# Kernel optimization log

Hardware: AMD Instinct MI355X
Metric: run time of the kernel (lower is better)

The kernel has to match this reference:

```python
import jax, jax.numpy as jnp
import numpy as np

B, S, D = 4, 2048, 1024
P = 2
N_FEAT = 16          # n_feature_know
N_REST = 16          # n_restore_know
R = 128              # knowledge_rank
D_SPACE = 64


def setup_inputs() -> dict:
    key = jax.random.key(0)
    ks = jax.random.split(key, 6)
    x = jax.random.normal(ks[0], (B, S, D), dtype=jnp.float32)
    # per-token routing weights for each of P feature paths, in [0,1)
    feature_paths = jax.random.uniform(ks[1], (P, B, S, N_FEAT), dtype=jnp.float32)
    f_know = jax.random.normal(ks[2], (N_FEAT, D, R), dtype=jnp.float32) * 0.02
    r_know = jax.random.normal(ks[3], (N_REST, R, D), dtype=jnp.float32) * 0.02
    feature_emb = jax.random.normal(ks[4], (N_FEAT, D_SPACE), dtype=jnp.float32)
    W_router = jax.random.normal(ks[5], (D_SPACE + R, N_REST), dtype=jnp.float32) * 0.05
    return {"x": x, "feature_paths": feature_paths, "f_know": f_know,
            "r_know": r_know, "feature_emb": feature_emb, "W_router": W_router}


def reference(x, feature_paths, f_know, r_know, feature_emb, W_router):
    # Feature projection into all N low-rank banks: [B,S,N,R]
    all_h = jnp.einsum('bsd,ndr->bsnr', x, f_know)
    # Weighted sum over banks per path: [P,B,S,R]
    h_all = jnp.einsum('bsnr,pbsn->pbsr', all_h, feature_paths)
    # Context for restore routing: [P,B,S,D_SPACE]
    neuron_ctx = jnp.einsum('pbsn,nd->pbsd', feature_paths, feature_emb)
    # restore_input = cat([neuron_ctx, h]) -> router -> softmax restore weights
    restore_input = jnp.concatenate([neuron_ctx, h_all], axis=-1)  # [P,B,S,D_SPACE+R]
    logits = jnp.einsum('pbsc,cn->pbsn', restore_input, W_router)
    w = jax.nn.softmax(logits, axis=-1)                            # [P,B,S,N_REST]
    # Restore + per-token weighted combine, summed over P paths: [B,S,D]
    output = jnp.einsum('pbsr,nrd,pbsn->bsd', h_all, r_know, w)
    restore_aux_loss = jnp.float32(0.0)
    return output, restore_aux_loss
```

## Files before the change

kernel.cpp:

```cpp
#include <hip/hip_runtime.h>

typedef __attribute__((ext_vector_type(4))) float f32x4;
typedef __bf16 bf16x8 __attribute__((ext_vector_type(8)));
typedef unsigned short ushort_t;

#define T_TOK 8192
#define DIM   1024
#define NRCOL 2048

#define VMW(n)  asm volatile("s_waitcnt vmcnt(" #n ")" ::: "memory")
#define SB0()   __builtin_amdgcn_sched_barrier(0)
#define BAR()   __builtin_amdgcn_s_barrier()

static __device__ __forceinline__ unsigned short f2bf(float f) {
  unsigned int u = __builtin_bit_cast(unsigned int, f);
  u += 0x7fffu + ((u >> 16) & 1u);
  return (unsigned short)(u >> 16);
}
static __device__ __forceinline__ float bfbits2f(unsigned int lo16) {
  return __builtin_bit_cast(float, lo16 << 16);
}
static __device__ __forceinline__ void gload16(const void* g, void* l) {
  __builtin_amdgcn_global_load_lds((const __attribute__((address_space(1))) void*)g,
                                   (__attribute__((address_space(3))) void*)l, 16, 0, 0);
}

__global__ __launch_bounds__(256) void prep_kernel(const float* __restrict__ x,
                                                   const float* __restrict__ fk,
                                                   const float* __restrict__ rk,
                                                   unsigned short* __restrict__ Xbf,
                                                   unsigned short* __restrict__ W1t,
                                                   unsigned short* __restrict__ W2t) {
  const int bid = blockIdx.x, tid = threadIdx.x;
  if (bid < 2048) {
    const float4* in4 = (const float4*)x;
    uint2* o4 = (uint2*)Xbf;
    #pragma unroll
    for (int it = 0; it < 4; ++it) {
      const int i = bid * 256 + tid + it * 524288;
      float4 v = in4[i];
      uint2 o;
      o.x = (unsigned)f2bf(v.x) | ((unsigned)f2bf(v.y) << 16);
      o.y = (unsigned)f2bf(v.z) | ((unsigned)f2bf(v.w) << 16);
      o4[i] = o;
    }
    return;
  }
  __shared__ float tile[32][33];
  const float* src;
  unsigned short* dst;
  int rows, cols, r0, c0;
  if (bid < 4096) {
    const int b = bid - 2048;
    const int z = b >> 7, rem = b & 127;
    src = fk + (size_t)z * 1024 * 128;
    dst = W1t + (size_t)z * 128 * 1024;
    rows = 1024; cols = 128;
    c0 = (rem & 3) * 32; r0 = (rem >> 2) * 32;
  } else {
    const int b = bid - 4096;
    src = rk; dst = W2t;
    rows = 2048; cols = 1024;
    c0 = (b & 31) * 32; r0 = (b >> 5) * 32;
  }
  const int tx = tid & 31, ty = tid >> 5;
  #pragma unroll
  for (int i = 0; i < 32; i += 8)
    tile[ty + i][tx] = src[(size_t)(r0 + ty + i) * cols + c0 + tx];
  __syncthreads();
  #pragma unroll
  for (int i = 0; i < 32; i += 8)
    dst[(size_t)(c0 + ty + i) * rows + r0 + tx] = f2bf(tile[tx][ty + i]);
}

template<int K, bool OUT_BF16>
__global__ __launch_bounds__(256, 2) void gemmD(const ushort_t* __restrict__ A,
                                                const ushort_t* __restrict__ Bt,
                                                void* __restrict__ Cp, int N) {
  constexpr int nt = K / 64;
  __shared__ ushort_t As[2][128 * 64];
  __shared__ ushort_t Bs[2][128 * 64];

  const int tid = threadIdx.x;
  const int nx = gridDim.x;
  const int orig = blockIdx.y * nx + blockIdx.x;
  const int q = (nx * gridDim.y) >> 3;
  const int swz = (orig & 7) * q + (orig >> 3);
  const int bx = swz % nx, by = swz / nx;

  const int lane = tid & 63, wv = tid >> 6;
  const int wm = wv >> 1, wn = wv & 1;
  const int lrow = lane & 15, lk = lane >> 4;

  const ushort_t* Ab = A + (size_t)by * 128 * K;
  const ushort_t* Bb = Bt + (size_t)bx * 128 * K;

  const int srow = tid >> 3;
  const int sch = (tid & 7) ^ (srow & 7);
  const ushort_t* pA[4];
  const ushort_t* pB[4];
  #pragma unroll
  for (int r = 0; r < 4; ++r) {
    pA[r] = Ab + (size_t)(r * 32 + srow) * K + sch * 8;
    pB[r] = Bb + (size_t)(r * 32 + srow) * K + sch * 8;
  }
  const int dL = tid * 8;

  auto stage = [&](int s, int adv) {
    #pragma unroll
    for (int r = 0; r < 4; ++r) gload16(pA[r] + adv, (void*)&As[s][r * 2048 + dL]);
    #pragma unroll
    for (int r = 0; r < 4; ++r) gload16(pB[r] + adv, (void*)&Bs[s][r * 2048 + dL]);
  };

  int oA[4], oB[4];
  #pragma unroll
  for (int m = 0; m < 4; ++m) {
    const int r = wm * 64 + m * 16 + lrow;
    oA[m] = r * 64 + (lk ^ (r & 7)) * 8;
  }
  #pragma unroll
  for (int n = 0; n < 4; ++n) {
    const int r = wn * 64 + n * 16 + lrow;
    oB[n] = r * 64 + (lk ^ (r & 7)) * 8;
  }

  f32x4 acc[4][4];
  #pragma unroll
  for (int m = 0; m < 4; ++m)
    #pragma unroll
    for (int n = 0; n < 4; ++n)
      acc[m][n] = (f32x4){0.f, 0.f, 0.f, 0.f};

  stage(0, 0);
  VMW(0); SB0(); BAR(); SB0();

  #pragma unroll
  for (int t = 0; t < nt; ++t) {
    const int s = t & 1;
    if (t + 1 < nt) stage(s ^ 1, (t + 1) * 64);
    #pragma unroll
    for (int ks = 0; ks < 2; ++ks) {
      bf16x8 av[4], bv[4];
      #pragma unroll
      for (int m = 0; m < 4; ++m) av[m] = *(const bf16x8*)&As[s][oA[m] ^ (ks * 32)];
      #pragma unroll
      for (int n = 0; n < 4; ++n) bv[n] = *(const bf16x8*)&Bs[s][oB[n] ^ (ks * 32)];
      __builtin_amdgcn_s_setprio(1);
      #pragma unroll
      for (int m = 0; m < 4; ++m)
        #pragma unroll
        for (int n = 0; n < 4; ++n)
          acc[m][n] = __builtin_amdgcn_mfma_f32_16x16x32_bf16(av[m], bv[n], acc[m][n], 0, 0, 0);
      __builtin_amdgcn_s_setprio(0);
    }
    SB0();
    if (t + 1 < nt) VMW(0);
    BAR(); SB0();
  }

  #pragma unroll
  for (int m = 0; m < 4; ++m) {
    const int row0 = by * 128 + wm * 64 + m * 16 + lk * 4;
    #pragma unroll
    for (int n = 0; n < 4; ++n) {
      const int col = bx * 128 + wn * 64 + n * 16 + lrow;
      #pragma unroll
      for (int j = 0; j < 4; ++j) {
        const size_t idx = (size_t)(row0 + j) * N + col;
        if constexpr (OUT_BF16) ((ushort_t*)Cp)[idx] = f2bf(acc[m][n][j]);
        else                    ((float*)Cp)[idx] = acc[m][n][j];
      }
    }
  }
}

__global__ __launch_bounds__(256) void middle_kernel(const unsigned short* __restrict__ AH,
                                                     const float* __restrict__ fp,
                                                     const float* __restrict__ femb,
                                                     const float* __restrict__ Wr,
                                                     unsigned short* __restrict__ Mout,
                                                     float* __restrict__ auxout) {
  __shared__ float G[16][16];
  __shared__ float WrBs[128 * 16];
  __shared__ float hs[4][2][128];
  __shared__ float wsm[4][2][16];
  const int tid = threadIdx.x;
  {
    const int n = tid >> 4, j = tid & 15;
    float s = 0.f;
    #pragma unroll
    for (int ds = 0; ds < 64; ++ds) s += femb[n * 64 + ds] * Wr[ds * 16 + j];
    G[n][j] = s;
    #pragma unroll
    for (int k = 0; k < 8; ++k)
      WrBs[tid * 8 + k] = Wr[64 * 16 + tid * 8 + k];
  }
  const int wv = tid >> 6, l = tid & 63;
  const int t = blockIdx.x * 4 + wv;

  float p0[16], p1[16];
  #pragma unroll
  for (int n = 0; n < 16; ++n) {
    p0[n] = fp[t * 16 + n];
    p1[n] = fp[T_TOK * 16 + t * 16 + n];
  }

  float h00 = 0.f, h01 = 0.f, h10 = 0.f, h11 = 0.f;
  const unsigned short* ahrow = AH + (size_t)t * NRCOL;
  #pragma unroll
  for (int n = 0; n < 16; ++n) {
    const unsigned int v = *(const unsigned int*)(ahrow + n * 128 + 2 * l);
    const float a0 = bfbits2f(v & 0xffffu);
    const float a1 = bfbits2f(v >> 16);
    h00 += a0 * p0[n]; h01 += a1 * p0[n];
    h10 += a0 * p1[n]; h11 += a1 * p1[n];
  }
  hs[wv][0][2 * l] = h00; hs[wv][0][2 * l + 1] = h01;
  hs[wv][1][2 * l] = h10; hs[wv][1][2 * l + 1] = h11;
  __syncthreads();

  {
    const int p = l >> 5, seg = (l >> 4) & 1, j = l & 15;
    const float* hp = hs[wv][p] + seg * 64;
    const float* wb = WrBs + seg * 64 * 16 + j;
    float s0 = 0.f, s1 = 0.f, s2 = 0.f, s3 = 0.f;
    #pragma unroll
    for (int r = 0; r < 64; r += 4) {
      s0 += hp[r]     * wb[(r)     * 16];
      s1 += hp[r + 1] * wb[(r + 1) * 16];
      s2 += hp[r + 2] * wb[(r + 2) * 16];
      s3 += hp[r + 3] * wb[(r + 3) * 16];
    }
    float s = (s0 + s1) + (s2 + s3);
    s += __shfl_xor(s, 16, 64);
    #pragma unroll
    for (int n = 0; n < 16; ++n) {
      const float fv = p ? p1[n] : p0[n];
      s += fv * G[n][j];
    }
    float mx = s;
    #pragma unroll
    for (int d = 1; d < 16; d <<= 1) mx = fmaxf(mx, __shfl_xor(mx, d, 64));
    const float e = __expf(s - mx);
    float sum = e;
    #pragma unroll
    for (int d = 1; d < 16; d <<= 1) sum += __shfl_xor(sum, d, 64);
    if (seg == 0) wsm[wv][p][j] = e / sum;
  }
  __syncthreads();

  unsigned short* mrow = Mout + (size_t)t * NRCOL;
  #pragma unroll
  for (int n = 0; n < 16; ++n) {
    const float w0 = wsm[wv][0][n], w1 = wsm[wv][1][n];
    const float m0 = w0 * h00 + w1 * h10;
    const float m1 = w0 * h01 + w1 * h11;
    const unsigned int pk = (unsigned)f2bf(m0) | ((unsigned)f2bf(m1) << 16);
    *(unsigned int*)(mrow + n * 128 + 2 * l) = pk;
  }
  if (blockIdx.x == 0 && tid == 0) auxout[0] = 0.f;
}

extern "C" void kernel_launch(void* const* d_in, const int* in_sizes, int n_in,
                              void* d_out, int out_size, void* d_ws, size_t ws_size,
                              hipStream_t stream) {
  const float* x    = (const float*)d_in[0];
  const float* fp   = (const float*)d_in[1];
  const float* fk   = (const float*)d_in[2];
  const float* rk   = (const float*)d_in[3];
  const float* femb = (const float*)d_in[4];
  const float* Wr   = (const float*)d_in[5];
  float* out = (float*)d_out;

  char* ws = (char*)d_ws;
  unsigned short* Xbf = (unsigned short*)ws;
  unsigned short* W1t = (unsigned short*)(ws + 16u * 1024 * 1024);
  unsigned short* Mb  = (unsigned short*)ws;
  unsigned short* W2t = (unsigned short*)(ws + 32u * 1024 * 1024);
  unsigned short* AH  = (unsigned short*)(ws + 36u * 1024 * 1024);

  prep_kernel<<<6144, 256, 0, stream>>>(x, fk, rk, Xbf, W1t, W2t);
  gemmD<1024, true><<<dim3(NRCOL / 128, T_TOK / 128), 256, 0, stream>>>(Xbf, W1t, AH, NRCOL);
  middle_kernel<<<T_TOK / 4, 256, 0, stream>>>(AH, fp, femb, Wr, Mb, out + 8388608);
  gemmD<2048, false><<<dim3(DIM / 128, T_TOK / 128), 256, 0, stream>>>(Mb, W2t, out, DIM);
}
```

Baseline: 107.7 us.

## Replace double-buffered GEMM with single-buffered load-then-compute loop

Converts both bf16 GEMMs from a double-buffered LDS pipeline, where the next tile is prefetched during MFMA compute, to a single-buffered loop that loads a tile, waits, computes, then barriers. It also drops the setprio hints, the occupancy hint in launch bounds, and full loop unrolling. This halves LDS use and may allow more resident blocks, but it exposes global load latency on every K-step because loads no longer overlap compute.

```diff
diff --git a/kernel.cpp b/kernel.cpp
--- a/kernel.cpp
+++ b/kernel.cpp
@@ -74,12 +74,12 @@
 }
 
 template<int K, bool OUT_BF16>
-__global__ __launch_bounds__(256, 2) void gemmD(const ushort_t* __restrict__ A,
-                                                const ushort_t* __restrict__ Bt,
-                                                void* __restrict__ Cp, int N) {
+__global__ __launch_bounds__(256) void gemmS(const ushort_t* __restrict__ A,
+                                             const ushort_t* __restrict__ Bt,
+                                             void* __restrict__ Cp, int N) {
   constexpr int nt = K / 64;
-  __shared__ ushort_t As[2][128 * 64];
-  __shared__ ushort_t Bs[2][128 * 64];
+  __shared__ ushort_t As[128 * 64];
+  __shared__ ushort_t Bs[128 * 64];
 
   const int tid = threadIdx.x;
   const int nx = gridDim.x;
@@ -106,13 +106,6 @@
   }
   const int dL = tid * 8;
 
-  auto stage = [&](int s, int adv) {
-    #pragma unroll
-    for (int r = 0; r < 4; ++r) gload16(pA[r] + adv, (void*)&As[s][r * 2048 + dL]);
-    #pragma unroll
-    for (int r = 0; r < 4; ++r) gload16(pB[r] + adv, (void*)&Bs[s][r * 2048 + dL]);
-  };
-
   int oA[4], oB[4];
   #pragma unroll
   for (int m = 0; m < 4; ++m) {
@@ -132,30 +125,28 @@
     for (int n = 0; n < 4; ++n)
       acc[m][n] = (f32x4){0.f, 0.f, 0.f, 0.f};
 
-  stage(0, 0);
-  VMW(0); SB0(); BAR(); SB0();
-
-  #pragma unroll
+  #pragma unroll 1
   for (int t = 0; t < nt; ++t) {
-    const int s = t & 1;
-    if (t + 1 < nt) stage(s ^ 1, (t + 1) * 64);
+    #pragma unroll
+    for (int r = 0; r < 4; ++r) gload16(pA[r] + t * 64, (void*)&As[r * 2048 + dL]);
+    #pragma unroll
+    for (int r = 0; r < 4; ++r) gload16(pB[r] + t * 64, (void*)&Bs[r * 2048 + dL]);
+    VMW(0); SB0();
+    BAR(); SB0();
     #pragma unroll
     for (int ks = 0; ks < 2; ++ks) {
       bf16x8 av[4], bv[4];
       #pragma unroll
-      for (int m = 0; m < 4; ++m) av[m] = *(const bf16x8*)&As[s][oA[m] ^ (ks * 32)];
-      #pragma unroll
-      for (int n = 0; n < 4; ++n) bv[n] = *(const bf16x8*)&Bs[s][oB[n] ^ (ks * 32)];
-      __builtin_amdgcn_s_setprio(1);
+      for (int m = 0; m < 4; ++m) av[m] = *(const bf16x8*)&As[oA[m] ^ (ks * 32)];
+      #pragma unroll
+      for (int n = 0; n < 4; ++n) bv[n] = *(const bf16x8*)&Bs[oB[n] ^ (ks * 32)];
       #pragma unroll
       for (int m = 0; m < 4; ++m)
         #pragma unroll
         for (int n = 0; n < 4; ++n)
           acc[m][n] = __builtin_amdgcn_mfma_f32_16x16x32_bf16(av[m], bv[n], acc[m][n], 0, 0, 0);
-      __builtin_amdgcn_s_setprio(0);
     }
     SB0();
-    if (t + 1 < nt) VMW(0);
     BAR(); SB0();
   }
 
@@ -281,7 +272,7 @@
   unsigned short* AH  = (unsigned short*)(ws + 36u * 1024 * 1024);
 
   prep_kernel<<<6144, 256, 0, stream>>>(x, fk, rk, Xbf, W1t, W2t);
-  gemmD<1024, true><<<dim3(NRCOL / 128, T_TOK / 128), 256, 0, stream>>>(Xbf, W1t, AH, NRCOL);
+  gemmS<1024, true><<<dim3(NRCOL / 128, T_TOK / 128), 256, 0, stream>>>(Xbf, W1t, AH, NRCOL);
   middle_kernel<<<T_TOK / 4, 256, 0, stream>>>(AH, fp, femb, Wr, Mb, out + 8388608);
-  gemmD<2048, false><<<dim3(DIM / 128, T_TOK / 128), 256, 0, stream>>>(Mb, W2t, out, DIM);
-}
+  gemmS<2048, false><<<dim3(DIM / 128, T_TOK / 128), 256, 0, stream>>>(Mb, W2t, out, DIM);
+}
```

Result: slower. 120.2 us (+11.6%).

## Fuse fp32-to-bf16 conversion of x into the first GEMM's A-tile loading

Applied to the files above, without the earlier changes.

The separate pass that converted x to bf16 in the prep kernel is removed. A new GEMM kernel instead loads fp32 x tiles into registers, packs them to bf16 and writes them into swizzled LDS, while B still streams directly to LDS. This removes a full read of x plus a write and re-read of the bf16 copy. In exchange, each column block of the GEMM now re-reads A at fp32 width, which doubles A-side traffic. A also passes through registers rather than using direct global-to-LDS loads, which adds register pressure and conversion ALU work inside the main loop.

```diff
diff --git a/kernel.cpp b/kernel.cpp
--- a/kernel.cpp
+++ b/kernel.cpp
@@ -2,12 +2,14 @@
 
 typedef __attribute__((ext_vector_type(4))) float f32x4;
 typedef __bf16 bf16x8 __attribute__((ext_vector_type(8)));
+typedef unsigned int u32x4 __attribute__((ext_vector_type(4)));
 typedef unsigned short ushort_t;
 
 #define T_TOK 8192
 #define DIM   1024
 #define NRCOL 2048
 
+#define LGKM0() asm volatile("s_waitcnt lgkmcnt(0)" ::: "memory")
 #define VMW(n)  asm volatile("s_waitcnt vmcnt(" #n ")" ::: "memory")
 #define SB0()   __builtin_amdgcn_sched_barrier(0)
 #define BAR()   __builtin_amdgcn_s_barrier()
@@ -17,6 +19,9 @@
   u += 0x7fffu + ((u >> 16) & 1u);
   return (unsigned short)(u >> 16);
 }
+static __device__ __forceinline__ unsigned pk2(float a, float b) {
+  return (unsigned)f2bf(a) | ((unsigned)f2bf(b) << 16);
+}
 static __device__ __forceinline__ float bfbits2f(unsigned int lo16) {
   return __builtin_bit_cast(float, lo16 << 16);
 }
@@ -25,40 +30,23 @@
                                    (__attribute__((address_space(3))) void*)l, 16, 0, 0);
 }
 
-__global__ __launch_bounds__(256) void prep_kernel(const float* __restrict__ x,
-                                                   const float* __restrict__ fk,
+__global__ __launch_bounds__(256) void prep_kernel(const float* __restrict__ fk,
                                                    const float* __restrict__ rk,
-                                                   unsigned short* __restrict__ Xbf,
                                                    unsigned short* __restrict__ W1t,
                                                    unsigned short* __restrict__ W2t) {
   const int bid = blockIdx.x, tid = threadIdx.x;
-  if (bid < 2048) {
-    const float4* in4 = (const float4*)x;
-    uint2* o4 = (uint2*)Xbf;
-    #pragma unroll
-    for (int it = 0; it < 4; ++it) {
-      const int i = bid * 256 + tid + it * 524288;
-      float4 v = in4[i];
-      uint2 o;
-      o.x = (unsigned)f2bf(v.x) | ((unsigned)f2bf(v.y) << 16);
-      o.y = (unsigned)f2bf(v.z) | ((unsigned)f2bf(v.w) << 16);
-      o4[i] = o;
-    }
-    return;
-  }
   __shared__ float tile[32][33];
   const float* src;
   unsigned short* dst;
   int rows, cols, r0, c0;
-  if (bid < 4096) {
-    const int b = bid - 2048;
-    const int z = b >> 7, rem = b & 127;
+  if (bid < 2048) {
+    const int z = bid >> 7, rem = bid & 127;
     src = fk + (size_t)z * 1024 * 128;
     dst = W1t + (size_t)z * 128 * 1024;
     rows = 1024; cols = 128;
     c0 = (rem & 3) * 32; r0 = (rem >> 2) * 32;
   } else {
-    const int b = bid - 4096;
+    const int b = bid - 2048;
     src = rk; dst = W2t;
     rows = 2048; cols = 1024;
     c0 = (b & 31) * 32; r0 = (b >> 5) * 32;
@@ -71,6 +59,126 @@
   #pragma unroll
   for (int i = 0; i < 32; i += 8)
     dst[(size_t)(c0 + ty + i) * rows + r0 + tx] = f2bf(tile[tx][ty + i]);
+}
+
+template<int K>
+__global__ __launch_bounds__(256, 2) void gemmX(const float* __restrict__ Af,
+                                                const ushort_t* __restrict__ Bt,
+                                                ushort_t* __restrict__ Cp, int N) {
+  constexpr int nt = K / 64;
+  __shared__ ushort_t As[2][128 * 64];
+  __shared__ ushort_t Bs[2][128 * 64];
+
+  const int tid = threadIdx.x;
+  const int nx = gridDim.x;
+  const int orig = blockIdx.y * nx + blockIdx.x;
+  const int q = (nx * gridDim.y) >> 3;
+  const int swz = (orig & 7) * q + (orig >> 3);
+  const int bx = swz % nx, by = swz / nx;
+
+  const int lane = tid & 63, wv = tid >> 6;
+  const int wm = wv >> 1, wn = wv & 1;
+  const int lrow = lane & 15, lk = lane >> 4;
+
+  const float* Ab = Af + (size_t)by * 128 * K;
+  const ushort_t* Bb = Bt + (size_t)bx * 128 * K;
+
+  const int srow = tid >> 3;
+  const int sch = (tid & 7) ^ (srow & 7);
+  const float* pAf[4];
+  const ushort_t* pB[4];
+  #pragma unroll
+  for (int r = 0; r < 4; ++r) {
+    pAf[r] = Ab + (size_t)(r * 32 + srow) * K + sch * 8;
+    pB[r]  = Bb + (size_t)(r * 32 + srow) * K + sch * 8;
+  }
+  const int dL = tid * 8;
+
+  auto stageB = [&](int s, int adv) {
+    #pragma unroll
+    for (int r = 0; r < 4; ++r) gload16(pB[r] + adv, (void*)&Bs[s][r * 2048 + dL]);
+  };
+  f32x4 va[8];
+  auto loadA = [&](int adv) {
+    #pragma unroll
+    for (int r = 0; r < 4; ++r) {
+      va[2 * r]     = *(const f32x4*)(pAf[r] + adv);
+      va[2 * r + 1] = *(const f32x4*)(pAf[r] + adv + 4);
+    }
+  };
+  auto writeA = [&](int s) {
+    #pragma unroll
+    for (int r = 0; r < 4; ++r) {
+      u32x4 o;
+      o[0] = pk2(va[2 * r][0], va[2 * r][1]);
+      o[1] = pk2(va[2 * r][2], va[2 * r][3]);
+      o[2] = pk2(va[2 * r + 1][0], va[2 * r + 1][1]);
+      o[3] = pk2(va[2 * r + 1][2], va[2 * r + 1][3]);
+      *(u32x4*)&As[s][r * 2048 + dL] = o;
+    }
+  };
+
+  int oA[4], oB[4];
+  #pragma unroll
+  for (int m = 0; m < 4; ++m) {
+    const int r = wm * 64 + m * 16 + lrow;
+    oA[m] = r * 64 + (lk ^ (r & 7)) * 8;
+  }
+  #pragma unroll
+  for (int n = 0; n < 4; ++n) {
+    const int r = wn * 64 + n * 16 + lrow;
+    oB[n] = r * 64 + (lk ^ (r & 7)) * 8;
+  }
+
+  f32x4 acc[4][4];
+  #pragma unroll
+  for (int m = 0; m < 4; ++m)
+    #pragma unroll
+    for (int n = 0; n < 4; ++n)
+      acc[m][n] = (f32x4){0.f, 0.f, 0.f, 0.f};
+
+  loadA(0);
+  stageB(0, 0);
+  writeA(0);
+  LGKM0(); VMW(0); SB0(); BAR(); SB0();
+
+  #pragma unroll
+  for (int t = 0; t < nt; ++t) {
+    const int s = t & 1;
+    if (t + 1 < nt) { loadA((t + 1) * 64); stageB(s ^ 1, (t + 1) * 64); }
+    #pragma unroll
+    for (int ks = 0; ks < 2; ++ks) {
+      bf16x8 av[4], bv[4];
+      #pragma unroll
+      for (int m = 0; m < 4; ++m) av[m] = *(const bf16x8*)&As[s][oA[m] ^ (ks * 32)];
+      #pragma unroll
+      for (int n = 0; n < 4; ++n) bv[n] = *(const bf16x8*)&Bs[s][oB[n] ^ (ks * 32)];
+      __builtin_amdgcn_s_setprio(1);
+      #pragma unroll
+      for (int m = 0; m < 4; ++m)
+        #pragma unroll
+        for (int n = 0; n < 4; ++n)
+          acc[m][n] = __builtin_amdgcn_mfma_f32_16x16x32_bf16(av[m], bv[n], acc[m][n], 0, 0, 0);
+      __builtin_amdgcn_s_setprio(0);
+    }
+    SB0();
+    if (t + 1 < nt) writeA(s ^ 1);
+    LGKM0();
+    if (t + 1 < nt) VMW(0);
+    BAR(); SB0();
+  }
+
+  #pragma unroll
+  for (int m = 0; m < 4; ++m) {
+    const int row0 = by * 128 + wm * 64 + m * 16 + lk * 4;
+    #pragma unroll
+    for (int n = 0; n < 4; ++n) {
+      const int col = bx * 128 + wn * 64 + n * 16 + lrow;
+      #pragma unroll
+      for (int j = 0; j < 4; ++j)
+        Cp[(size_t)(row0 + j) * N + col] = f2bf(acc[m][n][j]);
+    }
+  }
 }
 
 template<int K, bool OUT_BF16>
@@ -274,14 +382,13 @@
   float* out = (float*)d_out;
 
   char* ws = (char*)d_ws;
-  unsigned short* Xbf = (unsigned short*)ws;
+  unsigned short* Mb  = (unsigned short*)ws;
   unsigned short* W1t = (unsigned short*)(ws + 16u * 1024 * 1024);
-  unsigned short* Mb  = (unsigned short*)ws;
   unsigned short* W2t = (unsigned short*)(ws + 32u * 1024 * 1024);
   unsigned short* AH  = (unsigned short*)(ws + 36u * 1024 * 1024);
 
-  prep_kernel<<<6144, 256, 0, stream>>>(x, fk, rk, Xbf, W1t, W2t);
-  gemmD<1024, true><<<dim3(NRCOL / 128, T_TOK / 128), 256, 0, stream>>>(Xbf, W1t, AH, NRCOL);
+  prep_kernel<<<4096, 256, 0, stream>>>(fk, rk, W1t, W2t);
+  gemmX<1024><<<dim3(NRCOL / 128, T_TOK / 128), 256, 0, stream>>>(x, W1t, AH, NRCOL);
   middle_kernel<<<T_TOK / 4, 256, 0, stream>>>(AH, fp, femb, Wr, Mb, out + 8388608);
   gemmD<2048, false><<<dim3(DIM / 128, T_TOK / 128), 256, 0, stream>>>(Mb, W2t, out, DIM);
 }
```

New measurement: 116.3 us. 8.0% more time.
